# Optimization experiments

Hardware: AMD Instinct MI355X
Metric: run time of the kernel (lower is better)

The kernel has to match this reference:

```python
import jax, jax.numpy as jnp
import numpy as np

L = 8       # num_layers
D = 512     # embed_dim
H = 8       # num_heads
HD = D // H # head_dim = 64
V = 256     # vocab_size
T = 2048    # seq len (= context_length)
B = 4       # batch
FF = 4 * D  # mlp hidden
EPS = 1e-5


def setup_inputs() -> dict:
    key = jax.random.key(0)
    ks = jax.random.split(key, 18)
    g = lambda k, shape: (jax.random.normal(k, shape, jnp.float32) * 0.02)
    return {
        "x": jax.random.randint(ks[0], (B, T), 0, V),
        "tok_emb": g(ks[1], (V, D)),
        "pos_emb": g(ks[2], (T, D)),
        "attn_w": g(ks[3], (L, D, 3 * D)),
        "attn_b": g(ks[4], (L, 3 * D)),
        "proj_w": g(ks[5], (L, D, D)),
        "proj_b": g(ks[6], (L, D)),
        "ln1_g": jnp.ones((L, D), jnp.float32),
        "ln1_b": jnp.zeros((L, D), jnp.float32),
        "ln2_g": jnp.ones((L, D), jnp.float32),
        "ln2_b": jnp.zeros((L, D), jnp.float32),
        "ff1_w": g(ks[7], (L, D, FF)),
        "ff1_b": g(ks[8], (L, FF)),
        "ff2_w": g(ks[9], (L, FF, D)),
        "ff2_b": g(ks[10], (L, D)),
        "lnf_g": jnp.ones((D,), jnp.float32),
        "lnf_b": jnp.zeros((D,), jnp.float32),
    }


def _ln(x, g, b):
    m = jnp.mean(x, axis=-1, keepdims=True)
    v = jnp.mean(jnp.square(x - m), axis=-1, keepdims=True)
    return (x - m) * jax.lax.rsqrt(v + EPS) * g + b


def reference(x, tok_emb, pos_emb, attn_w, attn_b, proj_w, proj_b,
              ln1_g, ln1_b, ln2_g, ln2_b, ff1_w, ff1_b, ff2_w, ff2_b,
              lnf_g, lnf_b):
    Bx, Tx = x.shape
    h = tok_emb[x] + pos_emb[:Tx]                     # [B,T,D]
    causal = jnp.tril(jnp.ones((Tx, Tx), bool))       # [T,T]
    scale = 1.0 / np.sqrt(HD)
    for i in range(L):
        hn = _ln(h, ln1_g[i], ln1_b[i])
        qkv = hn @ attn_w[i] + attn_b[i]              # [B,T,3D]
        qkv = qkv.reshape(Bx, Tx, 3, H, HD)
        q = qkv[:, :, 0].transpose(0, 2, 1, 3)        # [B,H,T,HD]
        k = qkv[:, :, 1].transpose(0, 2, 1, 3)
        v = qkv[:, :, 2].transpose(0, 2, 1, 3)
        scores = jnp.einsum('bhqd,bhkd->bhqk', q, k) * scale
        scores = jnp.where(causal, scores, jnp.float32(-1e9))
        attn = jax.nn.softmax(scores, axis=-1)        # dropout identity at eval
        o = jnp.einsum('bhqk,bhkd->bhqd', attn, v)
        o = o.transpose(0, 2, 1, 3).reshape(Bx, Tx, D)
        h = h + o @ proj_w[i] + proj_b[i]
        hn2 = _ln(h, ln2_g[i], ln2_b[i])
        ff = jax.nn.gelu(hn2 @ ff1_w[i] + ff1_b[i], approximate=False)
        h = h + ff @ ff2_w[i] + ff2_b[i]
    logits = _ln(h, lnf_g, lnf_b) @ tok_emb.T         # tied lm_head
    return logits
```

## Files before the change

### kernel.cpp

```cpp
#include <hip/hip_runtime.h>

#define TT 2048
#define BB 4
#define DD 512
#define HH 8
#define LL 8
#define FFD 2048
#define VV 256
#define ROWS (BB*TT)

typedef short bf16x4 __attribute__((ext_vector_type(4)));
typedef short bf16x8 __attribute__((ext_vector_type(8)));
typedef float f32x4 __attribute__((ext_vector_type(4)));

#define GL2LDS(gp, lp) __builtin_amdgcn_global_load_lds( \
    (const __attribute__((address_space(1))) unsigned*)(gp), \
    (__attribute__((address_space(3))) unsigned*)(lp), 16, 0, 0)

__device__ __forceinline__ float bf2f(short s){
  union { unsigned u; float f; } x; x.u = ((unsigned)(unsigned short)s) << 16; return x.f;
}
__device__ __forceinline__ short f2bf(float f){
  union { float f; unsigned u; } x; x.f = f;
  unsigned r = (x.u + 0x7fffu + ((x.u >> 16) & 1u)) >> 16;
  return (short)(unsigned short)r;
}
__device__ __forceinline__ float ex2(float x){
  float r; asm("v_exp_f32 %0, %1" : "=v"(r) : "v"(x)); return r;
}
__device__ __forceinline__ unsigned cvtpk(float lo, float hi){
  unsigned r; asm("v_cvt_pk_bf16_f32 %0, %1, %2" : "=v"(r) : "v"(lo), "v"(hi)); return r;
}
__device__ __forceinline__ float xmax32(float x){ return fmaxf(x, __shfl_xor(x, 32)); }
__device__ __forceinline__ float xadd32(float x){ return x + __shfl_xor(x, 32); }

__device__ __forceinline__ float gelu_f(float v){
  float x = v * 0.70710678118f;
  float a = fabsf(x);
  float t = 1.0f / (1.0f + 0.3275911f * a);
  float poly = t*(0.254829592f + t*(-0.284496736f + t*(1.421413741f +
               t*(-1.453152027f + t*1.061405429f))));
  float er = 1.0f - poly * ex2(-1.44269504f * a * a);
  er = (x < 0.f) ? -er : er;
  return 0.5f * v * (1.0f + er);
}

__global__ __launch_bounds__(128) void embed_kernel(const int* __restrict__ x,
    const float* __restrict__ tok, const float* __restrict__ pos, float* __restrict__ h){
  int row = blockIdx.x;
  int t = row & (TT-1);
  int id = x[row];
  const float4 a = *(const float4*)&tok[(size_t)id*DD + threadIdx.x*4];
  const float4 p = *(const float4*)&pos[(size_t)t*DD + threadIdx.x*4];
  float4 r; r.x=a.x+p.x; r.y=a.y+p.y; r.z=a.z+p.z; r.w=a.w+p.w;
  *(float4*)&h[(size_t)row*DD + threadIdx.x*4] = r;
}

__global__ __launch_bounds__(256) void ln_kernel(const float* __restrict__ xx,
    const float* __restrict__ gw, const float* __restrict__ bw, short* __restrict__ out){
  const int lane = threadIdx.x & 63, w = threadIdx.x >> 6;
  const int row = blockIdx.x*4 + w;
  const float* xp = xx + (size_t)row*DD + lane*8;
  float4 a = *(const float4*)xp, c = *(const float4*)(xp+4);
  float xv[8] = {a.x,a.y,a.z,a.w,c.x,c.y,c.z,c.w};
  float s1 = 0.f, s2 = 0.f;
  #pragma unroll
  for (int e=0;e<8;e++){ s1 += xv[e]; s2 += xv[e]*xv[e]; }
  #pragma unroll
  for (int off=1; off<64; off<<=1){
    s1 += __shfl_xor(s1, off);
    s2 += __shfl_xor(s2, off);
  }
  const float m = s1 * (1.0f/DD);
  const float rstd = rsqrtf(s2*(1.0f/DD) - m*m + 1e-5f);
  const float4 g0 = *(const float4*)(gw + lane*8), g1 = *(const float4*)(gw + lane*8 + 4);
  const float4 b0 = *(const float4*)(bw + lane*8), b1 = *(const float4*)(bw + lane*8 + 4);
  float gg[8] = {g0.x,g0.y,g0.z,g0.w,g1.x,g1.y,g1.z,g1.w};
  float bb[8] = {b0.x,b0.y,b0.z,b0.w,b1.x,b1.y,b1.z,b1.w};
  short r[8];
  #pragma unroll
  for (int e=0;e<8;e++) r[e] = f2bf((xv[e]-m)*rstd*gg[e] + bb[e]);
  *(bf16x8*)&out[(size_t)row*DD + lane*8] = *(const bf16x8*)r;
}

__global__ __launch_bounds__(256) void transpose_cast_kernel(const float* __restrict__ src,
    short* __restrict__ dst, int R, int C){
  __shared__ float tile[32][33];
  size_t off = (size_t)blockIdx.z * R * C;
  src += off; dst += off;
  int c0 = blockIdx.x*32, r0 = blockIdx.y*32;
  int tx = threadIdx.x & 31, ty = threadIdx.x >> 5;
  #pragma unroll
  for (int i=0;i<4;i++) tile[ty + i*8][tx] = src[(size_t)(r0+ty+i*8)*C + c0 + tx];
  __syncthreads();
  #pragma unroll
  for (int i=0;i<4;i++) dst[(size_t)(c0+ty+i*8)*R + r0 + tx] = f2bf(tile[tx][ty+i*8]);
}

__global__ void cast_kernel(const float* __restrict__ in, short* __restrict__ out, int n){
  for (int i = blockIdx.x*blockDim.x + threadIdx.x; i < n; i += gridDim.x*blockDim.x)
    out[i] = f2bf(in[i]);
}

__device__ __forceinline__ void xcd_rowband(int gx, int gy, int& rowt, int& colt){
  int lin = blockIdx.y*gx + blockIdx.x;
  int x = lin & 7, j = lin >> 3;
  int jd = j / gy;
  rowt = x*(gx >> 3) + jd;
  colt = j - jd*gy;
}

template<int EPI>
__global__ __launch_bounds__(256) void gemm_dma(const short* __restrict__ A,
    const short* __restrict__ BT, const float* __restrict__ bias, void* __restrict__ C,
    int M, int N, int K)
{
  __shared__ short As[3][128*32];
  __shared__ short Bs[3][128*32];
  int rowt, colt;
  xcd_rowband(gridDim.x, gridDim.y, rowt, colt);
  const int row0 = rowt*128, col0 = colt*128;
  const int t = threadIdx.x, lane = t & 63, w = t >> 6;
  const int wm = w >> 1, wn = w & 1;
  const int rr = lane & 15, g = lane >> 4;
  f32x4 acc[4][4];
  #pragma unroll
  for (int m=0;m<4;m++)
    #pragma unroll
    for (int n=0;n<4;n++) acc[m][n] = (f32x4){0.f,0.f,0.f,0.f};

  const int srow = lane >> 2;
  const short* aP = A  + (size_t)(row0 + w*32 + srow)*K + (lane&3)*8;
  const short* bP = BT + (size_t)(col0 + w*32 + srow)*K + (lane&3)*8;

  const int nk = K >> 5;
  #pragma unroll
  for (int i=0;i<2;i++){
    GL2LDS(aP + (size_t)i*16*K, &As[0][w*1024 + i*512]);
    GL2LDS(bP + (size_t)i*16*K, &Bs[0][w*1024 + i*512]);
  }
  if (nk > 1){
    #pragma unroll
    for (int i=0;i<2;i++){
      GL2LDS(aP + (size_t)i*16*K + 32, &As[1][w*1024 + i*512]);
      GL2LDS(bP + (size_t)i*16*K + 32, &Bs[1][w*1024 + i*512]);
    }
  }
  int cur = 0, st = 2;
  for (int kt=0; kt<nk; kt++){
    if (kt < nk-1) asm volatile("s_waitcnt vmcnt(4) lgkmcnt(0)\n\ts_barrier" ::: "memory");
    else           asm volatile("s_waitcnt vmcnt(0) lgkmcnt(0)\n\ts_barrier" ::: "memory");
    if (kt+2 < nk){
      const int ko = (kt+2) << 5;
      #pragma unroll
      for (int i=0;i<2;i++){
        GL2LDS(aP + (size_t)i*16*K + ko, &As[st][w*1024 + i*512]);
        GL2LDS(bP + (size_t)i*16*K + ko, &Bs[st][w*1024 + i*512]);
      }
    }
    const short* Ac = As[cur];
    const short* Bc = Bs[cur];
    bf16x8 af[4], bfr[4];
    #pragma unroll
    for (int m=0;m<4;m++) af[m]  = *(const bf16x8*)&Ac[(wm*64 + m*16 + rr)*32 + g*8];
    #pragma unroll
    for (int n=0;n<4;n++) bfr[n] = *(const bf16x8*)&Bc[(wn*64 + n*16 + rr)*32 + g*8];
    #pragma unroll
    for (int m=0;m<4;m++)
      #pragma unroll
      for (int n=0;n<4;n++)
        acc[m][n] = __builtin_amdgcn_mfma_f32_16x16x32_bf16(af[m], bfr[n], acc[m][n], 0,0,0);
    cur = (cur==2) ? 0 : cur+1;
    st  = (st==2)  ? 0 : st+1;
  }
  #pragma unroll
  for (int m=0;m<4;m++){
    #pragma unroll
    for (int n=0;n<4;n++){
      int cg = col0 + wn*64 + n*16 + rr;
      float bv = bias[cg];
      #pragma unroll
      for (int i=0;i<4;i++){
        int rg = row0 + wm*64 + m*16 + g*4 + i;
        float v = acc[m][n][i] + bv;
        size_t idx = (size_t)rg*N + cg;
        if constexpr (EPI==1) ((short*)C)[idx] = f2bf(v);
        else if constexpr (EPI==2) ((short*)C)[idx] = f2bf(gelu_f(v));
        else ((float*)C)[idx] += v;
      }
    }
  }
}

__global__ __launch_bounds__(256) void gemm_dma_n64(const short* __restrict__ A,
    const short* __restrict__ BT, const float* __restrict__ bias, float* __restrict__ C,
    int M, int N, int K)
{
  __shared__ short As[128*64];
  __shared__ short Bs[64*64];
  int rowt, colt;
  xcd_rowband(gridDim.x, gridDim.y, rowt, colt);
  const int row0 = rowt*128, col0 = colt*64;
  const int t = threadIdx.x, lane = t & 63, w = t >> 6;
  const int wm = w >> 1, wn = w & 1;
  const int rr = lane & 15, g = lane >> 4;
  f32x4 acc[4][2];
  #pragma unroll
  for (int m=0;m<4;m++)
    #pragma unroll
    for (int n=0;n<2;n++) acc[m][n] = (f32x4){0.f,0.f,0.f,0.f};

  const short* aP = A  + (size_t)(row0 + w*32 + (lane>>3))*K + (lane&7)*8;
  const short* bP = BT + (size_t)(col0 + w*16 + (lane>>3))*K + (lane&7)*8;
  short* aL = As + w*2048;
  short* bL = Bs + w*1024;

  for (int kt=0; kt<K; kt+=64){
    __syncthreads();
    #pragma unroll
    for (int i=0;i<4;i++) GL2LDS(aP + (size_t)i*8*K + kt, aL + i*512);
    #pragma unroll
    for (int i=0;i<2;i++) GL2LDS(bP + (size_t)i*8*K + kt, bL + i*512);
    __syncthreads();
    #pragma unroll
    for (int ks=0; ks<2; ks++){
      bf16x8 af[4], bfr[2];
      #pragma unroll
      for (int m=0;m<4;m++) af[m]  = *(const bf16x8*)&As[(wm*64 + m*16 + rr)*64 + ks*32 + g*8];
      #pragma unroll
      for (int n=0;n<2;n++) bfr[n] = *(const bf16x8*)&Bs[(wn*32 + n*16 + rr)*64 + ks*32 + g*8];
      #pragma unroll
      for (int m=0;m<4;m++)
        #pragma unroll
        for (int n=0;n<2;n++)
          acc[m][n] = __builtin_amdgcn_mfma_f32_16x16x32_bf16(af[m], bfr[n], acc[m][n], 0,0,0);
    }
  }
  #pragma unroll
  for (int m=0;m<4;m++){
    #pragma unroll
    for (int n=0;n<2;n++){
      int cg = col0 + wn*32 + n*16 + rr;
      float bv = bias[cg];
      #pragma unroll
      for (int i=0;i<4;i++){
        int rg = row0 + wm*64 + m*16 + g*4 + i;
        C[(size_t)rg*N + cg] += acc[m][n][i] + bv;
      }
    }
  }
}

template<int BM, int BN>
__global__ __launch_bounds__(256) void gemm_small(const short* __restrict__ A,
    const short* __restrict__ BT, float* __restrict__ C, int M, int N, int K)
{
  constexpr int FM = BM/32, FN = BN/32;
  __shared__ short As[BM][72];
  __shared__ short Bs[BN][72];
  const int row0 = blockIdx.x*BM, col0 = blockIdx.y*BN;
  const int t = threadIdx.x, lane = t & 63, w = t >> 6;
  const int wm = w >> 1, wn = w & 1;
  const int rr = lane & 15, kg = (lane >> 4)*8;
  f32x4 acc[FM][FN];
  #pragma unroll
  for (int m=0;m<FM;m++)
    #pragma unroll
    for (int n=0;n<FN;n++) acc[m][n] = (f32x4){0.f,0.f,0.f,0.f};

  for (int kt=0; kt<K; kt+=64){
    #pragma unroll
    for (int i=0;i<BM/32;i++){
      int cid = t + i*256; int r = cid >> 3; int c = (cid & 7)*8;
      *(bf16x8*)&As[r][c] = *(const bf16x8*)&A[(size_t)(row0+r)*K + kt + c];
    }
    #pragma unroll
    for (int i=0;i<BN/32;i++){
      int cid = t + i*256; int r = cid >> 3; int c = (cid & 7)*8;
      *(bf16x8*)&Bs[r][c] = *(const bf16x8*)&BT[(size_t)(col0+r)*K + kt + c];
    }
    __syncthreads();
    #pragma unroll
    for (int ks=0; ks<2; ks++){
      bf16x8 af[FM], bfr[FN];
      #pragma unroll
      for (int m=0;m<FM;m++) af[m] = *(const bf16x8*)&As[wm*FM*16 + m*16 + rr][ks*32 + kg];
      #pragma unroll
      for (int n=0;n<FN;n++) bfr[n] = *(const bf16x8*)&Bs[wn*FN*16 + n*16 + rr][ks*32 + kg];
      #pragma unroll
      for (int m=0;m<FM;m++)
        #pragma unroll
        for (int n=0;n<FN;n++)
          acc[m][n] = __builtin_amdgcn_mfma_f32_16x16x32_bf16(af[m], bfr[n], acc[m][n], 0,0,0);
    }
    __syncthreads();
  }
  #pragma unroll
  for (int m=0;m<FM;m++)
    #pragma unroll
    for (int n=0;n<FN;n++){
      int cg = col0 + wn*FN*16 + n*16 + rr;
      #pragma unroll
      for (int i=0;i<4;i++){
        int rg = row0 + wm*FM*16 + m*16 + (lane>>4)*4 + i;
        C[(size_t)rg*N + cg] = acc[m][n][i];
      }
    }
}

__device__ __forceinline__ void attn_tile(const short* __restrict__ Kc,
    const short* __restrict__ Vc, const bf16x8* qr, f32x4* oacc,
    float& mrun, float& lpart, int qi, int g, int qloc, bool diag)
{
  f32x4 sacc[4];
  #pragma unroll
  for (int f=0; f<4; f++) sacc[f] = (f32x4){0.f,0.f,0.f,0.f};
  __builtin_amdgcn_s_setprio(1);
  #pragma unroll
  for (int ks=0; ks<2; ks++){
    #pragma unroll
    for (int f=0; f<4; f++){
      bf16x8 kf = *(const bf16x8*)&Kc[(f*16 + qi)*64 + (((ks*4 + g) ^ (qi&7))*8)];
      sacc[f] = __builtin_amdgcn_mfma_f32_16x16x32_bf16(kf, qr[ks], sacc[f], 0,0,0);
    }
  }
  __builtin_amdgcn_s_setprio(0);

  float p[4][4];
  if (diag){
    #pragma unroll
    for (int f=0; f<4; f++)
      #pragma unroll
      for (int i=0; i<4; i++){
        int koffs = f*16 + g*4 + i;
        p[f][i] = (koffs <= qloc) ? sacc[f][i] : -1e30f;
      }
  } else {
    #pragma unroll
    for (int f=0; f<4; f++)
      #pragma unroll
      for (int i=0; i<4; i++) p[f][i] = sacc[f][i];
  }
  float t0 = fmaxf(fmaxf(p[0][0],p[0][1]), fmaxf(p[0][2],p[0][3]));
  float t1 = fmaxf(fmaxf(p[1][0],p[1][1]), fmaxf(p[1][2],p[1][3]));
  float t2 = fmaxf(fmaxf(p[2][0],p[2][1]), fmaxf(p[2][2],p[2][3]));
  float t3 = fmaxf(fmaxf(p[3][0],p[3][1]), fmaxf(p[3][2],p[3][3]));
  float tm = fmaxf(fmaxf(t0,t1), fmaxf(t2,t3));
  tm = fmaxf(tm, __shfl_xor(tm, 16));
  tm = xmax32(tm);
  if (!__all(tm <= mrun + 8.f)){
    float mnew = fmaxf(mrun, tm);
    float corr = ex2(mrun - mnew);
    lpart *= corr;
    #pragma unroll
    for (int mf=0; mf<4; mf++)
      #pragma unroll
      for (int i=0; i<4; i++) oacc[mf][i] *= corr;
    mrun = mnew;
  }
  float ts = 0.f;
  #pragma unroll
  for (int f=0; f<4; f++)
    #pragma unroll
    for (int i=0; i<4; i++){
      float e = ex2(p[f][i] - mrun);
      p[f][i] = e;
      ts += e;
    }
  lpart += ts;

  __builtin_amdgcn_s_setprio(1);
  #pragma unroll
  for (int w2=0; w2<2; w2++){
    union { unsigned u[4]; bf16x8 v; } bfr;
    bfr.u[0] = cvtpk(p[2*w2  ][0], p[2*w2  ][1]);
    bfr.u[1] = cvtpk(p[2*w2  ][2], p[2*w2  ][3]);
    bfr.u[2] = cvtpk(p[2*w2+1][0], p[2*w2+1][1]);
    bfr.u[3] = cvtpk(p[2*w2+1][2], p[2*w2+1][3]);
    #pragma unroll
    for (int mf=0; mf<4; mf++){
      const short* vp = &Vc[(mf*16 + qi)*72 + w2*32 + g*4];
      union { bf16x4 h[2]; bf16x8 v; } af;
      af.h[0] = *(const bf16x4*)vp;
      af.h[1] = *(const bf16x4*)(vp + 16);
      oacc[mf] = __builtin_amdgcn_mfma_f32_16x16x32_bf16(af.v, bfr.v, oacc[mf], 0,0,0);
    }
  }
  __builtin_amdgcn_s_setprio(0);
}

__global__ __launch_bounds__(256) void attn_kernel(const short* __restrict__ qkv, short* __restrict__ o){
  __shared__ __align__(16) char smem[34816];
  short* KsB = (short*)smem;
  short* VtB = (short*)(smem + 16384);
  float* Osh = (float*)smem;

  const int lin = blockIdx.x;
  const int xcd = lin & 7, idx = lin >> 3;
  const int bh = xcd*4 + (idx & 3);
  const int qp = idx >> 2;
  const int b = bh >> 3, hh = bh & 7;
  const int ql = qp, qh = 31 - qp;
  const int nt = qh + 1;

  const int t = threadIdx.x, lane = t & 63, wid = t >> 6;
  const int g = lane >> 4, qi = lane & 15;
  const int qloc = wid*16 + qi;
  const size_t base = (size_t)b*TT*3*DD + hh*64;

  bf16x8 qL[2], qH[2];
  {
    const float qs = 0.125f * 1.44269504f;
    const short* qpL = qkv + base + (size_t)(ql*64 + qloc)*3*DD + g*8;
    const short* qpH = qkv + base + (size_t)(qh*64 + qloc)*3*DD + g*8;
    qL[0] = *(const bf16x8*)&qpL[0]; qL[1] = *(const bf16x8*)&qpL[32];
    qH[0] = *(const bf16x8*)&qpH[0]; qH[1] = *(const bf16x8*)&qpH[32];
    #pragma unroll
    for (int j=0;j<8;j++){
      qL[0][j] = f2bf(qs * bf2f(qL[0][j]));
      qL[1][j] = f2bf(qs * bf2f(qL[1][j]));
      qH[0][j] = f2bf(qs * bf2f(qH[0][j]));
      qH[1][j] = f2bf(qs * bf2f(qH[1][j]));
    }
  }
  f32x4 oL[4], oH[4];
  #pragma unroll
  for (int mf=0; mf<4; mf++){ oL[mf] = (f32x4){0.f,0.f,0.f,0.f}; oH[mf] = (f32x4){0.f,0.f,0.f,0.f}; }
  float mL = -1e30f, lL = 0.f, mH = -1e30f, lH = 0.f;

  const short* ksrc = qkv + base + DD + (size_t)(wid*16 + (lane>>3))*3*DD
                      + (((lane&7) ^ (lane>>3))*8);
  const int vk = (t & 31)*2, vd = (t >> 5)*8;
  const short* vsrc = qkv + base + 2*DD + (size_t)vk*3*DD + vd;

  GL2LDS(ksrc, KsB + wid*1024);
  GL2LDS(ksrc + (size_t)8*3*DD, KsB + wid*1024 + 512);
  bf16x8 v0a = *(const bf16x8*)vsrc;
  bf16x8 v0b = *(const bf16x8*)(vsrc + 3*DD);
  bf16x8 vLoA = *(const bf16x8*)(vsrc + (size_t)64*3*DD);
  bf16x8 vLoB = *(const bf16x8*)(vsrc + (size_t)64*3*DD + 3*DD);
  asm volatile("s_waitcnt vmcnt(0)" ::: "memory");
  #pragma unroll
  for (int e=0;e<8;e++)
    *(unsigned*)&VtB[(vd+e)*72 + vk] =
        (unsigned)(unsigned short)v0a[e] | ((unsigned)(unsigned short)v0b[e] << 16);

  for (int kb = 0; kb < nt; kb++){
    asm volatile("s_waitcnt vmcnt(0) lgkmcnt(0)\n\ts_barrier" ::: "memory");
    bf16x8 vHiA = vLoA, vHiB = vLoB;
    if (kb+1 < nt){
      const size_t koff = (size_t)(kb+1)*64*3*DD;
      short* kd = KsB + ((kb+1)&1)*4096 + wid*1024;
      GL2LDS(ksrc + koff, kd);
      GL2LDS(ksrc + koff + (size_t)8*3*DD, kd + 512);
      short* Vn = VtB + ((kb+1)&1)*4608;
      #pragma unroll
      for (int e=0;e<8;e++)
        *(unsigned*)&Vn[(vd+e)*72 + vk] =
            (unsigned)(unsigned short)vLoA[e] | ((unsigned)(unsigned short)vLoB[e] << 16);
    }
    if (kb+2 < nt){
      const size_t koff2 = (size_t)(kb+2)*64*3*DD;
      vHiA = *(const bf16x8*)(vsrc + koff2);
      vHiB = *(const bf16x8*)(vsrc + koff2 + 3*DD);
    }
    const short* Kc = KsB + (kb&1)*4096;
    const short* Vc = VtB + (kb&1)*4608;

    attn_tile(Kc, Vc, qH, oH, mH, lH, qi, g, qloc, kb == nt-1);
    if (kb <= ql)
      attn_tile(Kc, Vc, qL, oL, mL, lL, qi, g, qloc, kb == ql);

    vLoA = vHiA; vLoB = vHiB;
  }

  lL += __shfl_xor(lL, 16); lL = xadd32(lL);
  lH += __shfl_xor(lH, 16); lH = xadd32(lH);

  const int orow = t >> 2, cc = (t & 3) * 16;
  #pragma unroll
  for (int s=0; s<2; s++){
    const f32x4* oacc = s ? oH : oL;
    const float inv = 1.f / (s ? lH : lL);
    const int q0 = (s ? qh : ql) * 64;
    __syncthreads();
    #pragma unroll
    for (int mf=0; mf<4; mf++)
      #pragma unroll
      for (int i=0; i<4; i++)
        Osh[qloc*65 + mf*16 + g*4 + i] = oacc[mf][i] * inv;
    __syncthreads();
    short tmp[16];
    #pragma unroll
    for (int e=0; e<16; e++) tmp[e] = f2bf(Osh[orow*65 + cc + e]);
    short* op = o + ((size_t)b*TT + q0 + orow)*DD + hh*64 + cc;
    *(bf16x8*)&op[0] = *(const bf16x8*)&tmp[0];
    *(bf16x8*)&op[8] = *(const bf16x8*)&tmp[8];
  }
}

extern "C" void kernel_launch(void* const* d_in, const int* in_sizes, int n_in,
                              void* d_out, int out_size, void* d_ws, size_t ws_size,
                              hipStream_t stream) {
  const int*   x      = (const int*)d_in[0];
  const float* tok    = (const float*)d_in[1];
  const float* pos    = (const float*)d_in[2];
  const float* attn_w = (const float*)d_in[3];
  const float* attn_b = (const float*)d_in[4];
  const float* proj_w = (const float*)d_in[5];
  const float* proj_b = (const float*)d_in[6];
  const float* ln1_g  = (const float*)d_in[7];
  const float* ln1_b  = (const float*)d_in[8];
  const float* ln2_g  = (const float*)d_in[9];
  const float* ln2_b  = (const float*)d_in[10];
  const float* ff1_w  = (const float*)d_in[11];
  const float* ff1_b  = (const float*)d_in[12];
  const float* ff2_w  = (const float*)d_in[13];
  const float* ff2_b  = (const float*)d_in[14];
  const float* lnf_g  = (const float*)d_in[15];
  const float* lnf_b  = (const float*)d_in[16];

  char* p = (char*)d_ws;
  float* h   = (float*)p; p += (size_t)ROWS*DD*4;
  short* hn  = (short*)p; p += (size_t)ROWS*DD*2;
  short* qkv = (short*)p; p += (size_t)ROWS*3*DD*2;
  short* ob  = (short*)p; p += (size_t)ROWS*DD*2;
  short* ffb = (short*)p; p += (size_t)ROWS*FFD*2;
  short* awT = (short*)p; p += (size_t)LL*3*DD*DD*2;
  short* pwT = (short*)p; p += (size_t)LL*DD*DD*2;
  short* f1T = (short*)p; p += (size_t)LL*FFD*DD*2;
  short* f2T = (short*)p; p += (size_t)LL*DD*FFD*2;
  short* lmT = (short*)p; p += (size_t)VV*DD*2;

  transpose_cast_kernel<<<dim3(48,16,8),256,0,stream>>>(attn_w, awT, DD, 3*DD);
  transpose_cast_kernel<<<dim3(16,16,8),256,0,stream>>>(proj_w, pwT, DD, DD);
  transpose_cast_kernel<<<dim3(64,16,8),256,0,stream>>>(ff1_w, f1T, DD, FFD);
  transpose_cast_kernel<<<dim3(16,64,8),256,0,stream>>>(ff2_w, f2T, FFD, DD);
  cast_kernel<<<128,256,0,stream>>>(tok, lmT, VV*DD);
  embed_kernel<<<ROWS,128,0,stream>>>(x, tok, pos, h);

  for (int l=0;l<LL;l++){
    ln_kernel<<<ROWS/4,256,0,stream>>>(h, ln1_g + l*DD, ln1_b + l*DD, hn);
    gemm_dma<1><<<dim3(ROWS/128, (3*DD)/128),256,0,stream>>>(
        hn, awT + (size_t)l*3*DD*DD, attn_b + (size_t)l*3*DD, qkv, ROWS, 3*DD, DD);
    attn_kernel<<<512,256,0,stream>>>(qkv, ob);
    gemm_dma_n64<<<dim3(ROWS/128, DD/64),256,0,stream>>>(
        ob, pwT + (size_t)l*DD*DD, proj_b + (size_t)l*DD, h, ROWS, DD, DD);
    ln_kernel<<<ROWS/4,256,0,stream>>>(h, ln2_g + l*DD, ln2_b + l*DD, hn);
    gemm_dma<2><<<dim3(ROWS/128, FFD/128),256,0,stream>>>(
        hn, f1T + (size_t)l*FFD*DD, ff1_b + (size_t)l*FFD, ffb, ROWS, FFD, DD);
    gemm_dma_n64<<<dim3(ROWS/128, DD/64),256,0,stream>>>(
        ffb, f2T + (size_t)l*DD*FFD, ff2_b + (size_t)l*DD, h, ROWS, DD, FFD);
  }
  ln_kernel<<<ROWS/4,256,0,stream>>>(h, lnf_g, lnf_b, hn);
  gemm_small<64,64><<<dim3(ROWS/64, VV/64),256,0,stream>>>(
      hn, lmT, (float*)d_out, ROWS, VV, DD);
}
```

Before: 1.496 ms.

## Triple-buffer LDS in N64 residual GEMM with async global-to-LDS prefetch

Rewrites the gemm_dma_n64 main loop to use three LDS stages of K=32 tiles instead of a single K=64 tile. Loads are issued two stages ahead, and partial vmcnt waits plus a single barrier replace the two __syncthreads per iteration. The aim is to overlap global-memory latency with MFMA work. In exchange it halves the MFMA work per barrier, and it relies on hand-written waitcnt values matching the number of loads issued.

```diff
diff --git a/kernel.cpp b/kernel.cpp
--- a/kernel.cpp
+++ b/kernel.cpp
@@ -196,8 +196,8 @@
     const short* __restrict__ BT, const float* __restrict__ bias, float* __restrict__ C,
     int M, int N, int K)
 {
-  __shared__ short As[128*64];
-  __shared__ short Bs[64*64];
+  __shared__ short As[3][128*32];
+  __shared__ short Bs[3][64*32];
   int rowt, colt;
   xcd_rowband(gridDim.x, gridDim.y, rowt, colt);
   const int row0 = rowt*128, col0 = colt*64;
@@ -210,31 +210,43 @@
     #pragma unroll
     for (int n=0;n<2;n++) acc[m][n] = (f32x4){0.f,0.f,0.f,0.f};
 
-  const short* aP = A  + (size_t)(row0 + w*32 + (lane>>3))*K + (lane&7)*8;
-  const short* bP = BT + (size_t)(col0 + w*16 + (lane>>3))*K + (lane&7)*8;
-  short* aL = As + w*2048;
-  short* bL = Bs + w*1024;
-
-  for (int kt=0; kt<K; kt+=64){
-    __syncthreads();
-    #pragma unroll
-    for (int i=0;i<4;i++) GL2LDS(aP + (size_t)i*8*K + kt, aL + i*512);
-    #pragma unroll
-    for (int i=0;i<2;i++) GL2LDS(bP + (size_t)i*8*K + kt, bL + i*512);
-    __syncthreads();
-    #pragma unroll
-    for (int ks=0; ks<2; ks++){
-      bf16x8 af[4], bfr[2];
-      #pragma unroll
-      for (int m=0;m<4;m++) af[m]  = *(const bf16x8*)&As[(wm*64 + m*16 + rr)*64 + ks*32 + g*8];
-      #pragma unroll
-      for (int n=0;n<2;n++) bfr[n] = *(const bf16x8*)&Bs[(wn*32 + n*16 + rr)*64 + ks*32 + g*8];
-      #pragma unroll
-      for (int m=0;m<4;m++)
-        #pragma unroll
-        for (int n=0;n<2;n++)
-          acc[m][n] = __builtin_amdgcn_mfma_f32_16x16x32_bf16(af[m], bfr[n], acc[m][n], 0,0,0);
-    }
+  const int srow = lane >> 2;
+  const short* aP = A  + (size_t)(row0 + w*32 + srow)*K + (lane&3)*8;
+  const short* bP = BT + (size_t)(col0 + w*16 + srow)*K + (lane&3)*8;
+
+  const int nk = K >> 5;
+  #pragma unroll
+  for (int i=0;i<2;i++) GL2LDS(aP + (size_t)i*16*K, &As[0][w*1024 + i*512]);
+  GL2LDS(bP, &Bs[0][w*512]);
+  if (nk > 1){
+    #pragma unroll
+    for (int i=0;i<2;i++) GL2LDS(aP + (size_t)i*16*K + 32, &As[1][w*1024 + i*512]);
+    GL2LDS(bP + 32, &Bs[1][w*512]);
+  }
+  int cur = 0, st = 2;
+  for (int kt=0; kt<nk; kt++){
+    if (kt < nk-1) asm volatile("s_waitcnt vmcnt(3) lgkmcnt(0)\n\ts_barrier" ::: "memory");
+    else           asm volatile("s_waitcnt vmcnt(0) lgkmcnt(0)\n\ts_barrier" ::: "memory");
+    if (kt+2 < nk){
+      const int ko = (kt+2) << 5;
+      #pragma unroll
+      for (int i=0;i<2;i++) GL2LDS(aP + (size_t)i*16*K + ko, &As[st][w*1024 + i*512]);
+      GL2LDS(bP + ko, &Bs[st][w*512]);
+    }
+    const short* Ac = As[cur];
+    const short* Bc = Bs[cur];
+    bf16x8 af[4], bfr[2];
+    #pragma unroll
+    for (int m=0;m<4;m++) af[m]  = *(const bf16x8*)&Ac[(wm*64 + m*16 + rr)*32 + g*8];
+    #pragma unroll
+    for (int n=0;n<2;n++) bfr[n] = *(const bf16x8*)&Bc[(wn*32 + n*16 + rr)*32 + g*8];
+    #pragma unroll
+    for (int m=0;m<4;m++)
+      #pragma unroll
+      for (int n=0;n<2;n++)
+        acc[m][n] = __builtin_amdgcn_mfma_f32_16x16x32_bf16(af[m], bfr[n], acc[m][n], 0,0,0);
+    cur = (cur==2) ? 0 : cur+1;
+    st  = (st==2)  ? 0 : st+1;
   }
   #pragma unroll
   for (int m=0;m<4;m++){
```

After: 1.491 ms. Within noise of the previous version (-0.4%).
